# Kernel tuning notes

Hardware: AMD Instinct MI355X
Metric: run time of the kernel (lower is better)

Reference implementation:

```python
import jax, jax.numpy as jnp
import numpy as np

NUM_HEADS = 16


def setup_inputs() -> dict:
    key = jax.random.key(0)
    ks = jax.random.split(key, 11)
    S, E, F = 4096, 2048, 8192
    s = lambda k, shape, fan_in: jax.random.normal(k, shape, jnp.float32) / np.sqrt(fan_in)
    return {
        "emb": jax.random.normal(ks[0], (S, E), jnp.float32),
        "Wq": s(ks[1], (E, E), E), "bq": jnp.zeros((E,), jnp.float32),
        "Wk": s(ks[2], (E, E), E), "bk": jnp.zeros((E,), jnp.float32),
        "Wv": s(ks[3], (E, E), E), "bv": jnp.zeros((E,), jnp.float32),
        "W1": s(ks[4], (E, F), E), "b1": jnp.zeros((F,), jnp.float32),
        "W2": s(ks[5], (F, E), F), "b2": jnp.zeros((E,), jnp.float32),
    }


def reference(emb, Wq, bq, Wk, bk, Wv, bv, W1, b1, W2, b2):
    S, E = emb.shape
    H = NUM_HEADS
    D = E // H
    # project and split heads -> [H, S, D]
    q = (emb @ Wq + bq).reshape(S, H, D).transpose(1, 0, 2)
    k = (emb @ Wk + bk).reshape(S, H, D).transpose(1, 0, 2)
    v = (emb @ Wv + bv).reshape(S, H, D).transpose(1, 0, 2)
    scale = jnp.asarray(D, emb.dtype) ** 0.5
    scores = jnp.einsum("hsd,htd->hst", q, k) / scale  # [H, S, S]
    # causal mask: additive -1e9 strictly above the diagonal (matches torch.triu(..., 1)*-1e9)
    mask = jnp.triu(jnp.full((S, S), -1e9, dtype=scores.dtype), k=1)
    probs = jax.nn.softmax(scores + mask, axis=-1)
    attn = jnp.einsum("hst,htd->hsd", probs, v)  # [H, S, D]
    attn = attn.transpose(1, 0, 2).reshape(S, E)  # concat heads -> [S, E]
    hidden = jnp.maximum(attn @ W1 + b1, 0.0)
    return hidden @ W2 + b2
```

## Files before the change

### kernel.cpp

```cpp
#include <hip/hip_runtime.h>

typedef __attribute__((ext_vector_type(8))) short bf16x8;
typedef __attribute__((ext_vector_type(4))) float f32x4;
typedef __attribute__((ext_vector_type(8))) unsigned short u16x8;

static constexpr int S = 4096;
static constexpr int E = 2048;
static constexpr int F = 8192;
static constexpr int NH = 16;
static constexpr int DH = 128;

__device__ __forceinline__ unsigned short f2bf(float f) {
  unsigned u = __builtin_bit_cast(unsigned, f);
  u += 0x7FFFu + ((u >> 16) & 1u);
  return (unsigned short)(u >> 16);
}

__device__ __forceinline__ void async16(const unsigned short* g, unsigned short* l) {
  __builtin_amdgcn_global_load_lds(
      (const __attribute__((address_space(1))) unsigned int*)g,
      (__attribute__((address_space(3))) unsigned int*)l, 16, 0, 0);
}

__global__ __launch_bounds__(256) void cvt_bf16_kernel(const float* __restrict__ src,
                                                       unsigned short* __restrict__ dst) {
  int i = (blockIdx.x * 256 + threadIdx.x) * 4;
  float4 v = *(const float4*)(src + i);
  ushort4 o;
  o.x = f2bf(v.x); o.y = f2bf(v.y); o.z = f2bf(v.z); o.w = f2bf(v.w);
  *(ushort4*)(dst + i) = o;
}

__global__ __launch_bounds__(256) void transpose_cvt(const float* __restrict__ src,
                                                     unsigned short* __restrict__ dst,
                                                     const int Rr, const int Cc) {
  __shared__ float t[32][33];
  const int c0 = blockIdx.x * 32, r0 = blockIdx.y * 32;
  const int tx = threadIdx.x, ty = threadIdx.y;
#pragma unroll
  for (int i = 0; i < 4; ++i) {
    int r = ty + i * 8;
    t[r][tx] = src[(size_t)(r0 + r) * Cc + c0 + tx];
  }
  __syncthreads();
#pragma unroll
  for (int i = 0; i < 4; ++i) {
    int cr = ty + i * 8;
    dst[(size_t)(c0 + cr) * Rr + r0 + tx] = f2bf(t[tx][cr]);
  }
}

enum { EPI_QKV = 0, EPI_RELU = 1, EPI_OUT = 2 };

template <int EPI>
__global__ __launch_bounds__(256) void gemm_bt(
    const unsigned short* __restrict__ A, const unsigned short* __restrict__ B,
    const int K, const int N,
    const float* __restrict__ b0, const float* __restrict__ b1f, const float* __restrict__ b2f,
    unsigned short* __restrict__ o0, unsigned short* __restrict__ o1,
    unsigned short* __restrict__ o2, float* __restrict__ of) {
  __shared__ unsigned short lA[128 * 32];
  __shared__ unsigned short lB[128 * 32];
  const int tid = threadIdx.x, w = tid >> 6, lane = tid & 63;
  const int lane15 = lane & 15, l4 = lane >> 4;
  const int m0 = blockIdx.y * 128, n0 = blockIdx.x * 128;
  const int wr = w >> 1, wc = w & 1;

  const int u0 = (w * 2 + 0) * 64 + lane;
  const int u1 = (w * 2 + 1) * 64 + lane;
  const unsigned short* gA0 = A + (size_t)(m0 + (u0 >> 2)) * K + (u0 & 3) * 8;
  const unsigned short* gA1 = A + (size_t)(m0 + (u1 >> 2)) * K + (u1 & 3) * 8;
  const unsigned short* gB0 = B + (size_t)(n0 + (u0 >> 2)) * K + (u0 & 3) * 8;
  const unsigned short* gB1 = B + (size_t)(n0 + (u1 >> 2)) * K + (u1 & 3) * 8;
  unsigned short* dA0 = &lA[(w * 2 + 0) * 512];
  unsigned short* dA1 = &lA[(w * 2 + 1) * 512];
  unsigned short* dB0 = &lB[(w * 2 + 0) * 512];
  unsigned short* dB1 = &lB[(w * 2 + 1) * 512];

  const unsigned short* pa[4];
  const unsigned short* pb[4];
#pragma unroll
  for (int i = 0; i < 4; ++i) {
    pa[i] = &lA[(wr * 64 + i * 16 + lane15) * 32 + l4 * 8];
    pb[i] = &lB[(wc * 64 + i * 16 + lane15) * 32 + l4 * 8];
  }

  f32x4 zero4 = {0.f, 0.f, 0.f, 0.f};
  f32x4 acc[4][4];
#pragma unroll
  for (int i = 0; i < 4; ++i)
#pragma unroll
    for (int j = 0; j < 4; ++j) acc[i][j] = zero4;

  for (int ko = 0; ko < K; ko += 32) {
    __syncthreads();
    async16(gA0 + ko, dA0);
    async16(gA1 + ko, dA1);
    async16(gB0 + ko, dB0);
    async16(gB1 + ko, dB1);
    __syncthreads();
    bf16x8 av[4], bv[4];
#pragma unroll
    for (int i = 0; i < 4; ++i) av[i] = *(const bf16x8*)pa[i];
#pragma unroll
    for (int j = 0; j < 4; ++j) bv[j] = *(const bf16x8*)pb[j];
#pragma unroll
    for (int i = 0; i < 4; ++i)
#pragma unroll
      for (int j = 0; j < 4; ++j)
        acc[i][j] = __builtin_amdgcn_mfma_f32_16x16x32_bf16(av[i], bv[j], acc[i][j], 0, 0, 0);
  }

#pragma unroll
  for (int j = 0; j < 4; ++j) {
    const int n = n0 + wc * 64 + j * 16 + lane15;
    float bias;
    if (EPI == EPI_QKV)
      bias = (n < E) ? b0[n] : ((n < 2 * E) ? b1f[n - E] : b2f[n - 2 * E]);
    else
      bias = b0[n];
#pragma unroll
    for (int i = 0; i < 4; ++i) {
      const int mr = m0 + wr * 64 + i * 16 + l4 * 4;
      f32x4 v = acc[i][j];
#pragma unroll
      for (int r = 0; r < 4; ++r) {
        const float val = v[r] + bias;
        const int m = mr + r;
        if (EPI == EPI_QKV) {
          if (n < E)            o0[(size_t)m * E + n] = f2bf(val);
          else if (n < 2 * E)   o1[(size_t)m * E + (n - E)] = f2bf(val);
          else                  o2[(size_t)(n - 2 * E) * S + m] = f2bf(val);
        } else if (EPI == EPI_RELU) {
          o0[(size_t)m * N + n] = f2bf(fmaxf(val, 0.f));
        } else {
          of[(size_t)m * N + n] = val;
        }
      }
    }
  }
}

__global__ __launch_bounds__(256, 2) void flash_attn(const unsigned short* __restrict__ Qb,
                                                     const unsigned short* __restrict__ Kb,
                                                     const unsigned short* __restrict__ VTb,
                                                     unsigned short* __restrict__ attn) {
  const int qt = gridDim.x - 1 - blockIdx.x;
  const int h = blockIdx.y;
  const int qbase = qt * 64;
  const int tid = threadIdx.x, w = tid >> 6, lane = tid & 63;
  const int lane15 = lane & 15, l4 = lane >> 4;

  __shared__ unsigned short lK[2][64 * 128];
  __shared__ unsigned short lV[2][128 * 64];
  __shared__ unsigned short lP[4][16 * 72];

  bf16x8 aq[4];
  {
    const unsigned short* qrow = Qb + (size_t)(qbase + w * 16 + lane15) * E + h * DH + l4 * 8;
#pragma unroll
    for (int kk = 0; kk < 4; ++kk) aq[kk] = *(const bf16x8*)(qrow + kk * 32);
  }

  f32x4 zero4 = {0.f, 0.f, 0.f, 0.f};
  f32x4 o[8];
  float psum[4];
#pragma unroll
  for (int j = 0; j < 8; ++j) o[j] = zero4;
#pragma unroll
  for (int r = 0; r < 4; ++r) psum[r] = 0.f;

  {
#pragma unroll
    for (int i = 0; i < 4; ++i) {
      int c = i * 256 + w * 64 + lane;
      int row = c >> 4, pg = (c & 15) ^ (row & 15);
      async16(Kb + (size_t)row * E + h * DH + pg * 8, &lK[0][(i * 256 + w * 64) * 8]);
    }
#pragma unroll
    for (int i = 0; i < 4; ++i) {
      int c = i * 256 + w * 64 + lane;
      int row = c >> 3, pg = (c & 7) ^ (row & 7);
      async16(VTb + (size_t)(h * DH + row) * S + pg * 8, &lV[0][(i * 256 + w * 64) * 8]);
    }
  }

  const float scale = 0.088388347648318447f;

  for (int kt = 0; kt <= qt; ++kt) {
    __syncthreads();
    if (kt < qt) {
      const int kb2 = (kt + 1) * 64;
      const int nb = (kt + 1) & 1;
#pragma unroll
      for (int i = 0; i < 4; ++i) {
        int c = i * 256 + w * 64 + lane;
        int row = c >> 4, pg = (c & 15) ^ (row & 15);
        async16(Kb + (size_t)(kb2 + row) * E + h * DH + pg * 8, &lK[nb][(i * 256 + w * 64) * 8]);
      }
#pragma unroll
      for (int i = 0; i < 4; ++i) {
        int c = i * 256 + w * 64 + lane;
        int row = c >> 3, pg = (c & 7) ^ (row & 7);
        async16(VTb + (size_t)(h * DH + row) * S + kb2 + pg * 8, &lV[nb][(i * 256 + w * 64) * 8]);
      }
    }
    const int buf = kt & 1;

    f32x4 sacc[4];
#pragma unroll
    for (int j = 0; j < 4; ++j) sacc[j] = zero4;
#pragma unroll
    for (int kk = 0; kk < 4; ++kk)
#pragma unroll
      for (int j = 0; j < 4; ++j) {
        int pl = (kk * 4 + l4) ^ lane15;
        bf16x8 bk = *(const bf16x8*)&lK[buf][(j * 16 + lane15) * 128 + pl * 8];
        sacc[j] = __builtin_amdgcn_mfma_f32_16x16x32_bf16(aq[kk], bk, sacc[j], 0, 0, 0);
      }

    float p[4][4];
    if (kt == qt) {
#pragma unroll
      for (int j = 0; j < 4; ++j) {
        int col = j * 16 + lane15;
#pragma unroll
        for (int r = 0; r < 4; ++r) {
          int row = w * 16 + l4 * 4 + r;
          p[j][r] = (col <= row) ? __expf(sacc[j][r] * scale) : 0.f;
        }
      }
    } else {
#pragma unroll
      for (int j = 0; j < 4; ++j)
#pragma unroll
        for (int r = 0; r < 4; ++r) p[j][r] = __expf(sacc[j][r] * scale);
    }
#pragma unroll
    for (int r = 0; r < 4; ++r) psum[r] += p[0][r] + p[1][r] + p[2][r] + p[3][r];

#pragma unroll
    for (int j = 0; j < 4; ++j)
#pragma unroll
      for (int r = 0; r < 4; ++r)
        lP[w][(l4 * 4 + r) * 72 + j * 16 + lane15] = f2bf(p[j][r]);

#pragma unroll
    for (int ks = 0; ks < 2; ++ks) {
      bf16x8 ap = *(const bf16x8*)&lP[w][lane15 * 72 + ks * 32 + l4 * 8];
#pragma unroll
      for (int j = 0; j < 8; ++j) {
        int pl = (ks * 4 + l4) ^ (lane15 & 7);
        bf16x8 bv = *(const bf16x8*)&lV[buf][(j * 16 + lane15) * 64 + pl * 8];
        o[j] = __builtin_amdgcn_mfma_f32_16x16x32_bf16(ap, bv, o[j], 0, 0, 0);
      }
    }
  }

  float inv[4];
#pragma unroll
  for (int r = 0; r < 4; ++r) {
    float s = psum[r];
#pragma unroll
    for (int off = 1; off < 16; off <<= 1) s += __shfl_xor(s, off, 16);
    inv[r] = 1.0f / s;
  }
#pragma unroll
  for (int j = 0; j < 8; ++j)
#pragma unroll
    for (int r = 0; r < 4; ++r)
      attn[(size_t)(qbase + w * 16 + l4 * 4 + r) * E + h * DH + j * 16 + lane15] =
          f2bf(o[j][r] * inv[r]);
}

extern "C" void kernel_launch(void* const* d_in, const int* in_sizes, int n_in,
                              void* d_out, int out_size, void* d_ws, size_t ws_size,
                              hipStream_t stream) {
  (void)in_sizes; (void)n_in; (void)out_size; (void)ws_size;
  const float* emb = (const float*)d_in[0];
  const float* Wq  = (const float*)d_in[1];
  const float* bq  = (const float*)d_in[2];
  const float* Wk  = (const float*)d_in[3];
  const float* bk  = (const float*)d_in[4];
  const float* Wv  = (const float*)d_in[5];
  const float* bv  = (const float*)d_in[6];
  const float* W1  = (const float*)d_in[7];
  const float* b1  = (const float*)d_in[8];
  const float* W2  = (const float*)d_in[9];
  const float* b2  = (const float*)d_in[10];
  float* out = (float*)d_out;

  char* ws = (char*)d_ws;
  const size_t MB = 1024ull * 1024ull;
  unsigned short* embb   = (unsigned short*)(ws);
  unsigned short* attn   = embb;
  char* r1 = ws + 16 * MB;
  unsigned short* WqkvT  = (unsigned short*)(r1);
  unsigned short* Qb     = (unsigned short*)(r1 + 24 * MB);
  unsigned short* Kb     = (unsigned short*)(r1 + 40 * MB);
  unsigned short* VTb    = (unsigned short*)(r1 + 56 * MB);
  unsigned short* hidden = (unsigned short*)(r1);
  unsigned short* W1T    = (unsigned short*)(r1 + 72 * MB);
  unsigned short* W2T    = (unsigned short*)(r1 + 104 * MB);

  dim3 b256(256);
  dim3 tb(32, 8);
  cvt_bf16_kernel<<<dim3((S * E) / 1024), b256, 0, stream>>>(emb, embb);
  transpose_cvt<<<dim3(E / 32, E / 32), tb, 0, stream>>>(Wq, WqkvT, E, E);
  transpose_cvt<<<dim3(E / 32, E / 32), tb, 0, stream>>>(Wk, WqkvT + (size_t)E * E, E, E);
  transpose_cvt<<<dim3(E / 32, E / 32), tb, 0, stream>>>(Wv, WqkvT + 2ull * E * E, E, E);
  transpose_cvt<<<dim3(F / 32, E / 32), tb, 0, stream>>>(W1, W1T, E, F);
  transpose_cvt<<<dim3(E / 32, F / 32), tb, 0, stream>>>(W2, W2T, F, E);

  gemm_bt<EPI_QKV><<<dim3(3 * E / 128, S / 128), b256, 0, stream>>>(
      embb, WqkvT, E, 3 * E, bq, bk, bv, Qb, Kb, VTb, nullptr);
  flash_attn<<<dim3(S / 64, NH), b256, 0, stream>>>(Qb, Kb, VTb, attn);
  gemm_bt<EPI_RELU><<<dim3(F / 128, S / 128), b256, 0, stream>>>(
      attn, W1T, E, F, b1, nullptr, nullptr, hidden, nullptr, nullptr, nullptr);
  gemm_bt<EPI_OUT><<<dim3(E / 128, S / 128), b256, 0, stream>>>(
      hidden, W2T, F, E, b2, nullptr, nullptr, nullptr, nullptr, nullptr, out);
}
```

Baseline: 961.9 us.

## Double-buffer LDS tiles in bf16 GEMM to overlap global loads with MFMA

```diff
diff --git a/kernel.cpp b/kernel.cpp
--- a/kernel.cpp
+++ b/kernel.cpp
@@ -59,8 +59,8 @@
     const float* __restrict__ b0, const float* __restrict__ b1f, const float* __restrict__ b2f,
     unsigned short* __restrict__ o0, unsigned short* __restrict__ o1,
     unsigned short* __restrict__ o2, float* __restrict__ of) {
-  __shared__ unsigned short lA[128 * 32];
-  __shared__ unsigned short lB[128 * 32];
+  __shared__ unsigned short lA[2][128 * 32];
+  __shared__ unsigned short lB[2][128 * 32];
   const int tid = threadIdx.x, w = tid >> 6, lane = tid & 63;
   const int lane15 = lane & 15, l4 = lane >> 4;
   const int m0 = blockIdx.y * 128, n0 = blockIdx.x * 128;
@@ -72,18 +72,8 @@
   const unsigned short* gA1 = A + (size_t)(m0 + (u1 >> 2)) * K + (u1 & 3) * 8;
   const unsigned short* gB0 = B + (size_t)(n0 + (u0 >> 2)) * K + (u0 & 3) * 8;
   const unsigned short* gB1 = B + (size_t)(n0 + (u1 >> 2)) * K + (u1 & 3) * 8;
-  unsigned short* dA0 = &lA[(w * 2 + 0) * 512];
-  unsigned short* dA1 = &lA[(w * 2 + 1) * 512];
-  unsigned short* dB0 = &lB[(w * 2 + 0) * 512];
-  unsigned short* dB1 = &lB[(w * 2 + 1) * 512];
-
-  const unsigned short* pa[4];
-  const unsigned short* pb[4];
-#pragma unroll
-  for (int i = 0; i < 4; ++i) {
-    pa[i] = &lA[(wr * 64 + i * 16 + lane15) * 32 + l4 * 8];
-    pb[i] = &lB[(wc * 64 + i * 16 + lane15) * 32 + l4 * 8];
-  }
+  const int doff0 = (w * 2 + 0) * 512;
+  const int doff1 = (w * 2 + 1) * 512;
 
   f32x4 zero4 = {0.f, 0.f, 0.f, 0.f};
   f32x4 acc[4][4];
@@ -92,18 +82,28 @@
 #pragma unroll
     for (int j = 0; j < 4; ++j) acc[i][j] = zero4;
 
+  async16(gA0, &lA[0][doff0]);
+  async16(gA1, &lA[0][doff1]);
+  async16(gB0, &lB[0][doff0]);
+  async16(gB1, &lB[0][doff1]);
+
   for (int ko = 0; ko < K; ko += 32) {
     __syncthreads();
-    async16(gA0 + ko, dA0);
-    async16(gA1 + ko, dA1);
-    async16(gB0 + ko, dB0);
-    async16(gB1 + ko, dB1);
-    __syncthreads();
+    const int buf = (ko >> 5) & 1;
+    if (ko + 32 < K) {
+      const int nb = buf ^ 1;
+      async16(gA0 + ko + 32, &lA[nb][doff0]);
+      async16(gA1 + ko + 32, &lA[nb][doff1]);
+      async16(gB0 + ko + 32, &lB[nb][doff0]);
+      async16(gB1 + ko + 32, &lB[nb][doff1]);
+    }
     bf16x8 av[4], bv[4];
 #pragma unroll
-    for (int i = 0; i < 4; ++i) av[i] = *(const bf16x8*)pa[i];
-#pragma unroll
-    for (int j = 0; j < 4; ++j) bv[j] = *(const bf16x8*)pb[j];
+    for (int i = 0; i < 4; ++i)
+      av[i] = *(const bf16x8*)&lA[buf][(wr * 64 + i * 16 + lane15) * 32 + l4 * 8];
+#pragma unroll
+    for (int j = 0; j < 4; ++j)
+      bv[j] = *(const bf16x8*)&lB[buf][(wc * 64 + j * 16 + lane15) * 32 + l4 * 8];
 #pragma unroll
     for (int i = 0; i < 4; ++i)
 #pragma unroll
```

Measured after the change: 919.0 us. 1.05x faster.
